# Performance work log

Hardware: AMD Instinct MI355X
Metric: run time of the kernel (lower is better)

Reference implementation:

```python
import jax, jax.numpy as jnp
import numpy as np
import math

H = 16
D_MODEL = 1024
D_K = D_MODEL // H


def setup_inputs() -> dict:
    key = jax.random.key(0)
    ks = jax.random.split(key, 11)
    B, S = 2, 2048
    scale = 1.0 / math.sqrt(D_MODEL)
    inp = {
        "query": jax.random.normal(ks[0], (B, S, D_MODEL), dtype=jnp.float32),
        "key": jax.random.normal(ks[1], (B, S, D_MODEL), dtype=jnp.float32),
        "value": jax.random.normal(ks[2], (B, S, D_MODEL), dtype=jnp.float32),
        # torch nn.Linear convention: W is [out_features, in_features]
        "Wq": jax.random.normal(ks[3], (D_MODEL, D_MODEL), dtype=jnp.float32) * scale,
        "bq": jnp.zeros((D_MODEL,), dtype=jnp.float32),
        "Wk": jax.random.normal(ks[4], (D_MODEL, D_MODEL), dtype=jnp.float32) * scale,
        "bk": jnp.zeros((D_MODEL,), dtype=jnp.float32),
        "Wv": jax.random.normal(ks[5], (D_MODEL, D_MODEL), dtype=jnp.float32) * scale,
        "bv": jnp.zeros((D_MODEL,), dtype=jnp.float32),
        "Wo": jax.random.normal(ks[6], (D_MODEL, D_MODEL), dtype=jnp.float32) * scale,
        "bo": jnp.zeros((D_MODEL,), dtype=jnp.float32),
    }
    return inp


def _split_heads(x):
    # [b, s, h*d_k] -> [b, h, s, d_k]
    b, s, _ = x.shape
    return x.reshape(b, s, H, D_K).transpose(0, 2, 1, 3)


def reference(query, key, value, Wq, bq, Wk, bk, Wv, bv, Wo, bo):
    q = _split_heads(query @ Wq.T + bq)
    k = _split_heads(key @ Wk.T + bk)
    v = _split_heads(value @ Wv.T + bv)
    # scaled dot-product attention, full L x L scores per head
    scores = jnp.einsum("bhqd,bhkd->bhqk", q, k) / math.sqrt(D_K)
    attn = jax.nn.softmax(scores, axis=-1)
    ctx = jnp.einsum("bhqk,bhkd->bhqd", attn, v)  # [b, h, s, d_k]
    b, h, s, d = ctx.shape
    ctx = ctx.transpose(0, 2, 1, 3).reshape(b, s, h * d)
    return ctx @ Wo.T + bo
```

## Files before the change

### kernel.cpp

```cpp
#include <hip/hip_runtime.h>

typedef unsigned int u32;
typedef unsigned short u16;
typedef __attribute__((ext_vector_type(8))) short short8;
typedef __attribute__((ext_vector_type(4))) float f32x4;
typedef __attribute__((ext_vector_type(2))) u32 u32x2;
typedef __attribute__((ext_vector_type(4))) u32 u32x4;

#define DEV __device__ __forceinline__

DEV u16 f2bf(float f) {
  u32 u = __builtin_bit_cast(u32, f);
  u = (u + 0x7FFFu + ((u >> 16) & 1u)) >> 16;
  return (u16)u;
}

DEV float fexp2(float x) {
#if __has_builtin(__builtin_amdgcn_exp2f)
  return __builtin_amdgcn_exp2f(x);
#else
  return exp2f(x);
#endif
}

DEV u32 cvt_pk_bf16(float lo, float hi) {
  u32 r;
  asm("v_cvt_pk_bf16_f32 %0, %1, %2" : "=v"(r) : "v"(lo), "v"(hi));
  return r;
}

DEV void llds16(const void* g, void* lds) {
  __builtin_amdgcn_global_load_lds(
      (const __attribute__((address_space(1))) u32*)g,
      (__attribute__((address_space(3))) u32*)lds, 16, 0, 0);
}

struct CvtW {
  const float* src[4];
  u16* dst[4];
};

__global__ void cvt_w(CvtW cw) {
  int i = blockIdx.x * blockDim.x + threadIdx.x;
  int seg = i >> 17;
  size_t off = ((size_t)(i & 131071)) * 8;
  const f32x4* p = (const f32x4*)(cw.src[seg] + off);
  f32x4 a = p[0], b = p[1];
  u32x4 o;
  o[0] = cvt_pk_bf16(a[0], a[1]);
  o[1] = cvt_pk_bf16(a[2], a[3]);
  o[2] = cvt_pk_bf16(b[0], b[1]);
  o[3] = cvt_pk_bf16(b[2], b[3]);
  *(u32x4*)(cw.dst[seg] + off) = o;
}

struct GemmArgs {
  const void* A[3];
  const u16* W[3];
  const float* bias[3];
  void* C[3];
  float scale[3];
};

template <int BM, int BN, int WAVES_M, int OUT_BF16, int NB_M, int A_F32>
__global__ __launch_bounds__(256, 2) void gemm_bt(GemmArgs ga) {
  constexpr int K = 1024, N = 1024;
  constexpr int WAVES_N = 4 / WAVES_M;
  constexpr int WM = BM / WAVES_M, WN = BN / WAVES_N;
  constexpr int AM = WM / 16, AN = WN / 16;

  __shared__ u16 lsA[BM * 32];
  __shared__ u16 lsB[BN * 32];

  const u32 orig = blockIdx.x;
  const u32 nid = (orig & 7u) * (gridDim.x >> 3) + (orig >> 3);
  const int bn = (int)(nid & 7u);
  const int bm = (int)((nid >> 3) % (u32)NB_M);
  const int z = (int)((nid >> 3) / (u32)NB_M);

  const u16* __restrict__ W = ga.W[z];
  const int tid = threadIdx.x;
  const int l = tid & 63, w = tid >> 6;
  const int lg = l >> 4, lr = l & 15;
  const int wm = w / WAVES_N, wn = w % WAVES_N;

  f32x4 acc[AM][AN];
#pragma unroll
  for (int i = 0; i < AM; ++i)
#pragma unroll
    for (int j = 0; j < AN; ++j) acc[i][j] = (f32x4){0.f, 0.f, 0.f, 0.f};

#define WDMA_SWZ(NSEG)                                                          \
  {                                                                             \
    _Pragma("unroll") for (int i_ = 0; i_ < (NSEG); ++i_) {                     \
      u32 sb = (u32)(w * (NSEG) + i_) * 1024;                                   \
      u32 lbw = sb + l * 16;                                                    \
      u32 row = lbw >> 6;                                                       \
      u32 colB = (lbw & 63) ^ ((row & 3) << 4);                                 \
      llds16(W + (size_t)(bn * BN + row) * K + k0 + (colB >> 1),                \
             (char*)lsB + sb);                                                  \
    }                                                                           \
  }
#define FRAG_MFMA()                                                             \
  {                                                                             \
    short8 af[AM], bf[AN];                                                      \
    _Pragma("unroll") for (int i = 0; i < AM; ++i) {                            \
      u32 ar = (u32)(wm * WM + i * 16 + lr);                                    \
      af[i] = *(const short8*)((const char*)lsA + ar * 64 +                     \
                               ((u32)(lg * 16) ^ ((ar & 3) << 4)));             \
    }                                                                           \
    _Pragma("unroll") for (int j = 0; j < AN; ++j) {                            \
      u32 br = (u32)(wn * WN + j * 16 + lr);                                    \
      bf[j] = *(const short8*)((const char*)lsB + br * 64 +                     \
                               ((u32)(lg * 16) ^ ((br & 3) << 4)));             \
    }                                                                           \
    _Pragma("unroll") for (int i = 0; i < AM; ++i)                              \
    _Pragma("unroll") for (int j = 0; j < AN; ++j)                              \
      acc[i][j] = __builtin_amdgcn_mfma_f32_16x16x32_bf16(af[i], bf[j],         \
                                                          acc[i][j], 0, 0, 0); \
  }

  if constexpr (A_F32) {
    const float* __restrict__ Af = (const float*)ga.A[z];
    const u32 lb0 = (u32)(w * 2 + 0) * 1024 + l * 16;
    const u32 lb1 = (u32)(w * 2 + 1) * 1024 + l * 16;
    const u32 sw0 = lb0 ^ (((lb0 >> 6) & 3) << 4);
    const u32 sw1 = lb1 ^ (((lb1 >> 6) & 3) << 4);
    const float* src0 = Af + (size_t)(bm * BM + (lb0 >> 6)) * K + ((lb0 & 63) >> 1);
    const float* src1 = Af + (size_t)(bm * BM + (lb1 >> 6)) * K + ((lb1 & 63) >> 1);

    f32x4 cA0, cA1, cB0, cB1, nA0, nA1, nB0, nB1;
    cA0 = *(const f32x4*)src0; cA1 = *(const f32x4*)(src0 + 4);
    cB0 = *(const f32x4*)src1; cB1 = *(const f32x4*)(src1 + 4);

#define GSTEP(K0, CA0, CA1, CB0, CB1, NA0, NA1, NB0, NB1)                       \
  {                                                                             \
    const int k0 = (K0);                                                        \
    __syncthreads();                                                            \
    if (k0 + 32 < K) {          \
      NA0 = *(const f32x4*)(src0 + k0 + 32); NA1 = *(const f32x4*)(src0 + k0 + 36); \
      NB0 = *(const f32x4*)(src1 + k0 + 32); NB1 = *(const f32x4*)(src1 + k0 + 36); \
    }                                                                           \
    WDMA_SWZ(2);                                                                \
    {                                                                           \
      u32x4 o;                                                                  \
      o[0] = cvt_pk_bf16(CA0[0], CA0[1]); o[1] = cvt_pk_bf16(CA0[2], CA0[3]);   \
      o[2] = cvt_pk_bf16(CA1[0], CA1[1]); o[3] = cvt_pk_bf16(CA1[2], CA1[3]);   \
      *(u32x4*)((char*)lsA + sw0) = o;                                          \
      o[0] = cvt_pk_bf16(CB0[0], CB0[1]); o[1] = cvt_pk_bf16(CB0[2], CB0[3]);   \
      o[2] = cvt_pk_bf16(CB1[0], CB1[1]); o[3] = cvt_pk_bf16(CB1[2], CB1[3]);   \
      *(u32x4*)((char*)lsA + sw1) = o;                                          \
    }                                                                           \
    __syncthreads();                                                            \
    FRAG_MFMA();                                                                \
  }

    for (int kk = 0; kk < K; kk += 64) {
      GSTEP(kk, cA0, cA1, cB0, cB1, nA0, nA1, nB0, nB1);
      GSTEP(kk + 32, nA0, nA1, nB0, nB1, cA0, cA1, cB0, cB1);
    }
#undef GSTEP
  } else {
    const u16* __restrict__ A = (const u16*)ga.A[z];
    constexpr int SEGS = (BM + BN) / 16;
    constexpr int PW = SEGS / 4;
    for (int k0 = 0; k0 < K; k0 += 32) {
      __syncthreads();
#pragma unroll
      for (int i = 0; i < PW; ++i) {
        int s = w * PW + i;
        if (s < BM / 16) {
          u32 sb = s * 1024;
          u32 lb = sb + l * 16;
          u32 row = lb >> 6;
          u32 colB = (lb & 63) ^ ((row & 3) << 4);
          llds16(A + (size_t)(bm * BM + row) * K + k0 + (colB >> 1), (char*)lsA + sb);
        } else {
          u32 sb = (u32)(s - BM / 16) * 1024;
          u32 lb = sb + l * 16;
          u32 row = lb >> 6;
          u32 colB = (lb & 63) ^ ((row & 3) << 4);
          llds16(W + (size_t)(bn * BN + row) * K + k0 + (colB >> 1), (char*)lsB + sb);
        }
      }
      __syncthreads();
      FRAG_MFMA();
    }
  }
#undef WDMA_SWZ
#undef FRAG_MFMA

  const float sc = ga.scale[z];
  const float* __restrict__ bias = ga.bias[z];
#pragma unroll
  for (int j = 0; j < AN; ++j) {
    int col = bn * BN + wn * WN + j * 16 + lr;
    float bv = bias[col];
#pragma unroll
    for (int i = 0; i < AM; ++i) {
      int row0 = bm * BM + wm * WM + i * 16 + lg * 4;
#pragma unroll
      for (int r = 0; r < 4; ++r) {
        float v = (acc[i][j][r] + bv) * sc;
        if constexpr (OUT_BF16)
          ((u16*)ga.C[z])[(size_t)(row0 + r) * N + col] = f2bf(v);
        else
          ((float*)ga.C[z])[(size_t)(row0 + r) * N + col] = v;
      }
    }
  }
}

__global__ __launch_bounds__(256, 2) void attn_fwd(
    const u16* __restrict__ Q, const u16* __restrict__ Kp,
    const u16* __restrict__ V, u16* __restrict__ O) {
  constexpr int S = 2048, LD = 1024;
  __shared__ u16 Kt[4][64 * 64];
  __shared__ u16 Vt[4][64 * 64];
  const int tid = threadIdx.x;
  const int l = tid & 63, w = tid >> 6;
  const int lg = l >> 4, lr = l & 15;

  const u32 orig = blockIdx.x;
  const u32 nid = (orig & 7u) * 64u + (orig >> 3);
  const int qt = (int)(nid & 15u);
  const int h = (int)((nid >> 4) & 15u);
  const int b = (int)(nid >> 8);

  const size_t base = ((size_t)b * S) * LD + h * 64;
  const int q0 = qt * 128 + w * 32;

  short8 qf[2][2];
#pragma unroll
  for (int g = 0; g < 2; ++g)
#pragma unroll
    for (int c = 0; c < 2; ++c)
      qf[g][c] = *(const short8*)&Q[base + (size_t)(q0 + g * 16 + lr) * LD + c * 32 + lg * 8];

  f32x4 acc[2][4];
#pragma unroll
  for (int g = 0; g < 2; ++g)
#pragma unroll
    for (int i = 0; i < 4; ++i) acc[g][i] = (f32x4){0.f, 0.f, 0.f, 0.f};
  float lsum[2] = {0.f, 0.f};

  const int m = tid & 31;
  const int kp0 = m * 2;
  const int key0 = ((m & 16) << 1) + ((m & 2) << 3) + (((m >> 2) & 3) << 2) + ((m & 1) << 1);
  const int vd0 = (tid >> 5) * 8;

#define KSTAGE(T)                                                               \
  {                                                                             \
    _Pragma("unroll") for (int i_ = 0; i_ < 2; ++i_) {                          \
      u32 sb = (u32)(w * 2 + i_) * 1024;                                        \
      u32 lb = sb + l * 16;                                                     \
      u32 key = lb >> 7;                                                        \
      u32 inner = (lb & 127) ^ ((key & 7) << 4);                                \
      llds16(Kp + base + (size_t)((T) * 64 + key) * LD + (inner >> 1),          \
             (char*)Kt[(T) & 3] + sb);                                          \
    }                                                                           \
  }
#define VLOAD(T, VA, VB)                                                        \
  {                                                                             \
    VA = *(const short8*)&V[base + (size_t)((T) * 64 + key0) * LD + vd0];       \
    VB = *(const short8*)&V[base + (size_t)((T) * 64 + key0 + 1) * LD + vd0];   \
  }
#define VWRITE(T, VA, VB)                                                       \
  {                                                                             \
    _Pragma("unroll") for (int jj = 0; jj < 8; ++jj) {                          \
      u32 pv = (u32)(u16)(VA)[jj] | ((u32)(u16)(VB)[jj] << 16);                 \
      u32 addr = (u32)((vd0 + jj) * 128 + kp0 * 2) ^ ((u32)jj << 4);            \
      *(u32*)((char*)Vt[(T) & 3] + addr) = pv;                                  \
    }                                                                           \
  }
#define QK(T, SV)                                                               \
  {                                                                             \
    __builtin_amdgcn_s_setprio(1);                                              \
    _Pragma("unroll") for (int ks = 0; ks < 4; ++ks) {                          \
      u32 a0 = (u32)(((ks * 16 + lr) * 128 + lg * 16) ^ ((lr & 7) << 4));       \
      short8 kf0 = *(const short8*)((const char*)Kt[(T) & 3] + a0);             \
      short8 kf1 = *(const short8*)((const char*)Kt[(T) & 3] + (a0 ^ 64));      \
      _Pragma("unroll") for (int g = 0; g < 2; ++g) {                           \
        f32x4 s_ = (f32x4){0.f, 0.f, 0.f, 0.f};                                 \
        s_ = __builtin_amdgcn_mfma_f32_16x16x32_bf16(kf0, qf[g][0], s_, 0, 0, 0); \
        s_ = __builtin_amdgcn_mfma_f32_16x16x32_bf16(kf1, qf[g][1], s_, 0, 0, 0); \
        SV[g][ks] = s_;                                                         \
      }                                                                         \
    }                                                                           \
    __builtin_amdgcn_s_setprio(0);                                              \
  }
#define SM(SV, PK)                                                              \
  {                                                                             \
    _Pragma("unroll") for (int g = 0; g < 2; ++g) {                             \
      _Pragma("unroll") for (int ks = 0; ks < 4; ++ks) {                        \
        float e0 = fexp2(SV[g][ks][0]), e1 = fexp2(SV[g][ks][1]);               \
        float e2 = fexp2(SV[g][ks][2]), e3 = fexp2(SV[g][ks][3]);               \
        lsum[g] += (e0 + e1) + (e2 + e3);                                       \
        PK[g][ks * 2 + 0] = cvt_pk_bf16(e0, e1);                                \
        PK[g][ks * 2 + 1] = cvt_pk_bf16(e2, e3);                                \
      }                                                                         \
    }                                                                           \
  }
#define PV(T, PK)                                                               \
  {                                                                             \
    __builtin_amdgcn_s_setprio(1);                                              \
    _Pragma("unroll") for (int ds = 0; ds < 4; ++ds) {                          \
      _Pragma("unroll") for (int c = 0; c < 2; ++c) {                           \
        u32 va_ = (u32)(((ds * 16 + lr) * 128 + c * 64 + lg * 16) ^ ((lr & 7) << 4)); \
        short8 vf = *(const short8*)((const char*)Vt[(T) & 3] + va_);           \
        _Pragma("unroll") for (int g = 0; g < 2; ++g) {                         \
          u32x4 pc = {PK[g][c * 4 + 0], PK[g][c * 4 + 1], PK[g][c * 4 + 2], PK[g][c * 4 + 3]}; \
          short8 pf = __builtin_bit_cast(short8, pc);                           \
          acc[g][ds] = __builtin_amdgcn_mfma_f32_16x16x32_bf16(vf, pf, acc[g][ds], 0, 0, 0); \
        }                                                                       \
      }                                                                         \
    }                                                                           \
    __builtin_amdgcn_s_setprio(0);                                              \
  }
#define ITER(t, SVC, SVN, VCA, VCB, VNA, VNB)                                   \
  {                                                                             \
    if ((t) < 30) { VLOAD((t) + 2, VNA, VNB); KSTAGE((t) + 2); }                \
    if ((t) < 31) QK((t) + 1, SVN);                                             \
    u32 pk_[2][8];                                                              \
    SM(SVC, pk_);                                                               \
    if ((t) < 31) VWRITE((t) + 1, VCA, VCB);                                    \
    PV(t, pk_);                                                                 \
    __syncthreads();                                                            \
  }

  f32x4 svA[2][4], svB[2][4];
  short8 vaA, vbA, vaB, vbB;

  VLOAD(0, vaB, vbB); KSTAGE(0);
  VLOAD(1, vaA, vbA); KSTAGE(1);
  VWRITE(0, vaB, vbB);
  __syncthreads();
  QK(0, svA);

  for (int tt = 0; tt < 16; ++tt) {
    ITER(2 * tt, svA, svB, vaA, vbA, vaB, vbB);
    ITER(2 * tt + 1, svB, svA, vaB, vbB, vaA, vbA);
  }

#pragma unroll
  for (int g = 0; g < 2; ++g) {
    lsum[g] += __shfl_xor(lsum[g], 16);
    lsum[g] += __shfl_xor(lsum[g], 32);
  }
#pragma unroll
  for (int g = 0; g < 2; ++g) {
    float inv = __builtin_amdgcn_rcpf(lsum[g]);
#pragma unroll
    for (int ds = 0; ds < 4; ++ds) {
      u32x2 ov;
      ov[0] = cvt_pk_bf16(acc[g][ds][0] * inv, acc[g][ds][1] * inv);
      ov[1] = cvt_pk_bf16(acc[g][ds][2] * inv, acc[g][ds][3] * inv);
      *(u32x2*)&O[base + (size_t)(q0 + g * 16 + lr) * LD + ds * 16 + lg * 4] = ov;
    }
  }
#undef KSTAGE
#undef VLOAD
#undef VWRITE
#undef QK
#undef SM
#undef PV
#undef ITER
}

extern "C" void kernel_launch(void* const* d_in, const int* in_sizes, int n_in,
                              void* d_out, int out_size, void* d_ws, size_t ws_size,
                              hipStream_t stream) {
  constexpr size_t SZ_X = 4096ull * 1024;
  constexpr size_t SZ_W = 1024ull * 1024;
  const float* bq = (const float*)d_in[4];
  const float* bk = (const float*)d_in[6];
  const float* bv = (const float*)d_in[8];
  const float* bo = (const float*)d_in[10];

  char* ws = (char*)d_ws;
  u16* wqb = (u16*)ws;
  u16* wkb = wqb + SZ_W;
  u16* wvb = wkb + SZ_W;
  u16* wob = wvb + SZ_W;
  u16* Qp = wob + SZ_W;
  u16* Kp = Qp + SZ_X;
  u16* Vp = Kp + SZ_X;
  u16* Cx = Vp + SZ_X;

  CvtW cw;
  cw.src[0] = (const float*)d_in[3]; cw.dst[0] = wqb;
  cw.src[1] = (const float*)d_in[5]; cw.dst[1] = wkb;
  cw.src[2] = (const float*)d_in[7]; cw.dst[2] = wvb;
  cw.src[3] = (const float*)d_in[9]; cw.dst[3] = wob;
  cvt_w<<<dim3(2048), 256, 0, stream>>>(cw);

  GemmArgs g1;
  g1.A[0] = d_in[0]; g1.A[1] = d_in[1]; g1.A[2] = d_in[2];
  g1.W[0] = wqb; g1.W[1] = wkb; g1.W[2] = wvb;
  g1.bias[0] = bq; g1.bias[1] = bk; g1.bias[2] = bv;
  g1.C[0] = Qp; g1.C[1] = Kp; g1.C[2] = Vp;
  g1.scale[0] = 0.18033688011112042f;
  g1.scale[1] = 1.f; g1.scale[2] = 1.f;
  gemm_bt<128, 128, 2, 1, 32, 1><<<dim3(768), 256, 0, stream>>>(g1);

  attn_fwd<<<dim3(512), 256, 0, stream>>>(Qp, Kp, Vp, Cx);

  GemmArgs g2 = {};
  g2.A[0] = Cx; g2.W[0] = wob; g2.bias[0] = bo; g2.C[0] = d_out; g2.scale[0] = 1.f;
  gemm_bt<64, 128, 1, 0, 64, 0><<<dim3(512), 256, 0, stream>>>(g2);
}
```

Measured before the change: 123.6 us.

## Double-buffer LDS tiles in projection GEMM and drop XOR swizzle

Changes the projection GEMM to use two LDS buffers for the A and W tiles. The next k-slice is staged (global-to-LDS DMA plus the fp32-to-bf16 conversion) while MFMAs run on the current one, which cuts the barrier count per k-step from two to one. It also removes the XOR bank swizzle on LDS addresses, so plain row-major fragment reads may now hit bank conflicts. LDS use per block doubles, which could lower occupancy.

```diff
diff --git a/kernel.cpp b/kernel.cpp
--- a/kernel.cpp
+++ b/kernel.cpp
@@ -69,8 +69,8 @@
   constexpr int WM = BM / WAVES_M, WN = BN / WAVES_N;
   constexpr int AM = WM / 16, AN = WN / 16;
 
-  __shared__ u16 lsA[BM * 32];
-  __shared__ u16 lsB[BN * 32];
+  __shared__ u16 lsA[2][BM * 32];
+  __shared__ u16 lsB[2][BN * 32];
 
   const u32 orig = blockIdx.x;
   const u32 nid = (orig & 7u) * (gridDim.x >> 3) + (orig >> 3);
@@ -90,30 +90,22 @@
 #pragma unroll
     for (int j = 0; j < AN; ++j) acc[i][j] = (f32x4){0.f, 0.f, 0.f, 0.f};
 
-#define WDMA_SWZ(NSEG)                                                          \
-  {                                                                             \
-    _Pragma("unroll") for (int i_ = 0; i_ < (NSEG); ++i_) {                     \
-      u32 sb = (u32)(w * (NSEG) + i_) * 1024;                                   \
+#define WDMA(K0, LSX)                                                           \
+  {                                                                             \
+    _Pragma("unroll") for (int i_ = 0; i_ < BN / 64; ++i_) {                    \
+      u32 sb = (u32)(w * (BN / 64) + i_) * 1024;                                \
       u32 lbw = sb + l * 16;                                                    \
-      u32 row = lbw >> 6;                                                       \
-      u32 colB = (lbw & 63) ^ ((row & 3) << 4);                                 \
-      llds16(W + (size_t)(bn * BN + row) * K + k0 + (colB >> 1),                \
-             (char*)lsB + sb);                                                  \
-    }                                                                           \
-  }
-#define FRAG_MFMA()                                                             \
+      u32 row = lbw >> 6, colS = (lbw & 63) >> 1;                               \
+      llds16(W + (size_t)(bn * BN + row) * K + (K0) + colS, (char*)(LSX) + sb); \
+    }                                                                           \
+  }
+#define FRAG_MFMA(LA, LB)                                                       \
   {                                                                             \
     short8 af[AM], bf[AN];                                                      \
-    _Pragma("unroll") for (int i = 0; i < AM; ++i) {                            \
-      u32 ar = (u32)(wm * WM + i * 16 + lr);                                    \
-      af[i] = *(const short8*)((const char*)lsA + ar * 64 +                     \
-                               ((u32)(lg * 16) ^ ((ar & 3) << 4)));             \
-    }                                                                           \
-    _Pragma("unroll") for (int j = 0; j < AN; ++j) {                            \
-      u32 br = (u32)(wn * WN + j * 16 + lr);                                    \
-      bf[j] = *(const short8*)((const char*)lsB + br * 64 +                     \
-                               ((u32)(lg * 16) ^ ((br & 3) << 4)));             \
-    }                                                                           \
+    _Pragma("unroll") for (int i = 0; i < AM; ++i)                              \
+      af[i] = *(const short8*)&(LA)[(wm * WM + i * 16 + lr) * 32 + lg * 8];     \
+    _Pragma("unroll") for (int j = 0; j < AN; ++j)                              \
+      bf[j] = *(const short8*)&(LB)[(wn * WN + j * 16 + lr) * 32 + lg * 8];     \
     _Pragma("unroll") for (int i = 0; i < AM; ++i)                              \
     _Pragma("unroll") for (int j = 0; j < AN; ++j)                              \
       acc[i][j] = __builtin_amdgcn_mfma_f32_16x16x32_bf16(af[i], bf[j],         \
@@ -124,70 +116,84 @@
     const float* __restrict__ Af = (const float*)ga.A[z];
     const u32 lb0 = (u32)(w * 2 + 0) * 1024 + l * 16;
     const u32 lb1 = (u32)(w * 2 + 1) * 1024 + l * 16;
-    const u32 sw0 = lb0 ^ (((lb0 >> 6) & 3) << 4);
-    const u32 sw1 = lb1 ^ (((lb1 >> 6) & 3) << 4);
     const float* src0 = Af + (size_t)(bm * BM + (lb0 >> 6)) * K + ((lb0 & 63) >> 1);
     const float* src1 = Af + (size_t)(bm * BM + (lb1 >> 6)) * K + ((lb1 & 63) >> 1);
 
+#define ACVT(PA0, PA1, PB0, PB1, LSX)                                           \
+  {                                                                             \
+    u32x4 o;                                                                    \
+    o[0] = cvt_pk_bf16(PA0[0], PA0[1]); o[1] = cvt_pk_bf16(PA0[2], PA0[3]);     \
+    o[2] = cvt_pk_bf16(PA1[0], PA1[1]); o[3] = cvt_pk_bf16(PA1[2], PA1[3]);     \
+    *(u32x4*)((char*)(LSX) + lb0) = o;                                          \
+    o[0] = cvt_pk_bf16(PB0[0], PB0[1]); o[1] = cvt_pk_bf16(PB0[2], PB0[3]);     \
+    o[2] = cvt_pk_bf16(PB1[0], PB1[1]); o[3] = cvt_pk_bf16(PB1[2], PB1[3]);     \
+    *(u32x4*)((char*)(LSX) + lb1) = o;                                          \
+  }
+#define ALOAD(K0, PA0, PA1, PB0, PB1)                                           \
+  {                                                                             \
+    PA0 = *(const f32x4*)(src0 + (K0));     PA1 = *(const f32x4*)(src0 + (K0) + 4); \
+    PB0 = *(const f32x4*)(src1 + (K0));     PB1 = *(const f32x4*)(src1 + (K0) + 4); \
+  }
+
     f32x4 cA0, cA1, cB0, cB1, nA0, nA1, nB0, nB1;
-    cA0 = *(const f32x4*)src0; cA1 = *(const f32x4*)(src0 + 4);
-    cB0 = *(const f32x4*)src1; cB1 = *(const f32x4*)(src1 + 4);
-
-#define GSTEP(K0, CA0, CA1, CB0, CB1, NA0, NA1, NB0, NB1)                       \
-  {                                                                             \
-    const int k0 = (K0);                                                        \
-    __syncthreads();                                                            \
-    if (k0 + 32 < K) {          \
-      NA0 = *(const f32x4*)(src0 + k0 + 32); NA1 = *(const f32x4*)(src0 + k0 + 36); \
-      NB0 = *(const f32x4*)(src1 + k0 + 32); NB1 = *(const f32x4*)(src1 + k0 + 36); \
-    }                                                                           \
-    WDMA_SWZ(2);                                                                \
-    {                                                                           \
-      u32x4 o;                                                                  \
-      o[0] = cvt_pk_bf16(CA0[0], CA0[1]); o[1] = cvt_pk_bf16(CA0[2], CA0[3]);   \
-      o[2] = cvt_pk_bf16(CA1[0], CA1[1]); o[3] = cvt_pk_bf16(CA1[2], CA1[3]);   \
-      *(u32x4*)((char*)lsA + sw0) = o;                                          \
-      o[0] = cvt_pk_bf16(CB0[0], CB0[1]); o[1] = cvt_pk_bf16(CB0[2], CB0[3]);   \
-      o[2] = cvt_pk_bf16(CB1[0], CB1[1]); o[3] = cvt_pk_bf16(CB1[2], CB1[3]);   \
-      *(u32x4*)((char*)lsA + sw1) = o;                                          \
-    }                                                                           \
-    __syncthreads();                                                            \
-    FRAG_MFMA();                                                                \
-  }
+    WDMA(0, lsB[0]);
+    ALOAD(0, cA0, cA1, cB0, cB1);
+    ACVT(cA0, cA1, cB0, cB1, lsA[0]);
+    ALOAD(32, nA0, nA1, nB0, nB1);
+    __syncthreads();
 
     for (int kk = 0; kk < K; kk += 64) {
-      GSTEP(kk, cA0, cA1, cB0, cB1, nA0, nA1, nB0, nB1);
-      GSTEP(kk + 32, nA0, nA1, nB0, nB1, cA0, cA1, cB0, cB1);
+      if (kk + 32 < K) {
+        WDMA(kk + 32, lsB[1]);
+        ACVT(nA0, nA1, nB0, nB1, lsA[1]);
+      }
+      if (kk + 64 < K) ALOAD(kk + 64, cA0, cA1, cB0, cB1);
+      FRAG_MFMA(lsA[0], lsB[0]);
+      __syncthreads();
+      if (kk + 64 < K) {
+        WDMA(kk + 64, lsB[0]);
+        ACVT(cA0, cA1, cB0, cB1, lsA[0]);
+      }
+      if (kk + 96 < K) ALOAD(kk + 96, nA0, nA1, nB0, nB1);
+      FRAG_MFMA(lsA[1], lsB[1]);
+      __syncthreads();
     }
-#undef GSTEP
+#undef ACVT
+#undef ALOAD
   } else {
     const u16* __restrict__ A = (const u16*)ga.A[z];
     constexpr int SEGS = (BM + BN) / 16;
     constexpr int PW = SEGS / 4;
-    for (int k0 = 0; k0 < K; k0 += 32) {
+#define STAGE_ALL(K0, LA, LB)                                                   \
+  {                                                                             \
+    _Pragma("unroll") for (int i_ = 0; i_ < PW; ++i_) {                         \
+      int s = w * PW + i_;                                    \
+      if (s < BM / 16) {                                                        \
+        u32 sb = s * 1024;                                                      \
+        u32 lb = sb + l * 16;                                                   \
+        u32 row = lb >> 6, colS = (lb & 63) >> 1;                               \
+        llds16(A + (size_t)(bm * BM + row) * K + (K0) + colS, (char*)(LA) + sb); \
+      } else {                                                                  \
+        u32 sb = (u32)(s - BM / 16) * 1024;                                     \
+        u32 lb = sb + l * 16;                                                   \
+        u32 row = lb >> 6, colS = (lb & 63) >> 1;                               \
+        llds16(W + (size_t)(bn * BN + row) * K + (K0) + colS, (char*)(LB) + sb); \
+      }                                                                         \
+    }                                                                           \
+  }
+    STAGE_ALL(0, lsA[0], lsB[0]);
+    __syncthreads();
+    for (int kk = 0; kk < K; kk += 64) {
+      if (kk + 32 < K) STAGE_ALL(kk + 32, lsA[1], lsB[1]);
+      FRAG_MFMA(lsA[0], lsB[0]);
       __syncthreads();
-#pragma unroll
-      for (int i = 0; i < PW; ++i) {
-        int s = w * PW + i;
-        if (s < BM / 16) {
-          u32 sb = s * 1024;
-          u32 lb = sb + l * 16;
-          u32 row = lb >> 6;
-          u32 colB = (lb & 63) ^ ((row & 3) << 4);
-          llds16(A + (size_t)(bm * BM + row) * K + k0 + (colB >> 1), (char*)lsA + sb);
-        } else {
-          u32 sb = (u32)(s - BM / 16) * 1024;
-          u32 lb = sb + l * 16;
-          u32 row = lb >> 6;
-          u32 colB = (lb & 63) ^ ((row & 3) << 4);
-          llds16(W + (size_t)(bn * BN + row) * K + k0 + (colB >> 1), (char*)lsB + sb);
-        }
-      }
+      if (kk + 64 < K) STAGE_ALL(kk + 64, lsA[0], lsB[0]);
+      FRAG_MFMA(lsA[1], lsB[1]);
       __syncthreads();
-      FRAG_MFMA();
     }
-  }
-#undef WDMA_SWZ
+#undef STAGE_ALL
+  }
+#undef WDMA
 #undef FRAG_MFMA
 
   const float sc = ga.scale[z];
```

Result: faster. 118.3 us (-4.3%).
